# Optimization experiments

Measured on AMD Instinct MI355X. Metric: run time of the kernel, lower is better.

## Reference

```python
import jax, jax.numpy as jnp
import numpy as np

D = 512       # hidden_size (attention defaults hardcode 512)
N = 8         # num_heads
H = D // N    # depth per head = 64
FF = 2048     # FFN filter size (hardcoded)
EPS = 1e-6


def _layer_norm(x, gamma, beta):
    # matches functional layer_norm: biased variance, eps inside sqrt
    mean = jnp.mean(x, axis=-1, keepdims=True)
    var = jnp.mean((x - mean) ** 2, axis=-1, keepdims=True)
    return gamma * ((x - mean) / jnp.sqrt(var + EPS)) + beta


def setup_inputs() -> dict:
    key = jax.random.key(0)
    ks = jax.random.split(key, 12)
    B, S = 8, 1024
    s = lambda k, shape, scale: jax.random.normal(k, shape, jnp.float32) * scale
    return {
        "inputs": s(ks[0], (B, S, D), 1.0),
        "attention_bias": jnp.zeros((B, 1, 1, S), jnp.float32),
        "ln1_g": jnp.ones((D,), jnp.float32),
        "ln1_b": jnp.zeros((D,), jnp.float32),
        "wq": s(ks[1], (D, N, H), D ** -0.5),
        "wk": s(ks[2], (D, N, H), D ** -0.5),
        "wv": s(ks[3], (D, N, H), D ** -0.5),
        "wo": s(ks[4], (N, H, D), D ** -0.5),
        "ln2_g": jnp.ones((D,), jnp.float32),
        "ln2_b": jnp.zeros((D,), jnp.float32),
        "w1": s(ks[5], (D, FF), D ** -0.5),
        "b1": jnp.zeros((FF,), jnp.float32),
        "w2": s(ks[6], (FF, D), FF ** -0.5),
        "b2": jnp.zeros((D,), jnp.float32),
    }


def reference(inputs, attention_bias, ln1_g, ln1_b, wq, wk, wv, wo,
              ln2_g, ln2_b, w1, b1, w2, b2):
    # --- self-attention block (pre-LN, residual) ---
    y = _layer_norm(inputs, ln1_g, ln1_b)
    q = jnp.einsum('bsd,dnh->bsnh', y, wq) * (H ** -0.5)
    k = jnp.einsum('bsd,dnh->bsnh', y, wk)
    v = jnp.einsum('bsd,dnh->bsnh', y, wv)
    # logits[b,n,f,t] = sum_h k[b,t,n,h] * q[b,f,n,h]
    logits = jnp.einsum('btnh,bfnh->bnft', k, q) + attention_bias
    weights = jax.nn.softmax(logits, axis=3)
    attn = jnp.einsum('bnft,btnh->bfnh', weights, v)
    attn_out = jnp.einsum('bfnh,nhd->bfd', attn, wo)
    x = inputs + attn_out

    # --- FFN block (pre-LN, residual) ---
    y2 = _layer_norm(x, ln2_g, ln2_b)
    h = jax.nn.relu(jnp.einsum('bsd,df->bsf', y2, w1) + b1)
    ffn_out = jnp.einsum('bsf,fd->bsd', h, w2) + b2
    return x + ffn_out
```

## Files before the change

kernel.cpp:

```cpp
#include <hip/hip_runtime.h>
#include <stdint.h>

typedef unsigned short u16;
typedef __attribute__((ext_vector_type(8))) __bf16 bf16x8;
typedef __attribute__((ext_vector_type(2))) __bf16 bf16x2;
typedef __attribute__((ext_vector_type(4))) float f32x4;

__device__ __forceinline__ float bf2f(u16 u) {
    union { unsigned int i; float f; } c; c.i = ((unsigned int)u) << 16; return c.f;
}
__device__ __forceinline__ u16 f2bf_sw(float f) {
    union { float f; unsigned int i; } c; c.f = f;
    unsigned int u = c.i;
    u += 0x7FFFu + ((u >> 16) & 1u);
    return (u16)(u >> 16);
}
__device__ __forceinline__ unsigned f2bf2(float lo, float hi) {
#if __has_builtin(__builtin_amdgcn_cvt_pk_bf16_f32)
    union { bf16x2 v; unsigned u; } c;
    c.v = __builtin_amdgcn_cvt_pk_bf16_f32(lo, hi);
    return c.u;
#else
    return (unsigned)f2bf_sw(lo) | ((unsigned)f2bf_sw(hi) << 16);
#endif
}
__device__ __forceinline__ u16 f2bf(float f) {
#if __has_builtin(__builtin_amdgcn_cvt_pk_bf16_f32)
    return (u16)(f2bf2(f, 0.f) & 0xFFFFu);
#else
    return f2bf_sw(f);
#endif
}
__device__ __forceinline__ bool sniff_f32(const unsigned* probe) {
    return probe && ((*probe & 0xFFFFu) == 0u);
}
__device__ __forceinline__ float lde(const void* p, size_t i, bool isf32) {
    return isf32 ? ((const float*)p)[i] : bf2f(((const u16*)p)[i]);
}
__device__ __forceinline__ void g2lds16(const void* g, void* l) {
    __builtin_amdgcn_global_load_lds(
        (__attribute__((address_space(1))) void*)(uintptr_t)g,
        (__attribute__((address_space(3))) void*)(unsigned int)(uintptr_t)l,
        16, 0, 0);
}

__global__ void prep_weights(const void* __restrict__ wq, const void* __restrict__ wk,
                             const void* __restrict__ wv, const void* __restrict__ wo,
                             const void* __restrict__ w1, const void* __restrict__ w2,
                             u16* __restrict__ wqkvT, u16* __restrict__ woT,
                             u16* __restrict__ w1T, u16* __restrict__ w2T,
                             const unsigned* probe) {
    __shared__ u16 t[32][33];
    const bool isf32 = sniff_f32(probe);
    const int id = blockIdx.x;
    const void* src; u16* dst; int R, C, cb, rb; float scale = 1.f;
    if (id < 1024) {
        const int which = id >> 8, tl = id & 255;
        R = 512; C = 512; cb = (tl & 15) * 32; rb = (tl >> 4) * 32;
        if (which == 0)      { src = wq; dst = wqkvT;              scale = 0.125f; }
        else if (which == 1) { src = wk; dst = wqkvT + 512 * 512; }
        else if (which == 2) { src = wv; dst = wqkvT + 1024 * 512; }
        else                 { src = wo; dst = woT; }
    } else if (id < 2048) {
        const int tl = id - 1024; src = w1; dst = w1T; R = 512; C = 2048;
        cb = (tl & 63) * 32; rb = (tl >> 6) * 32;
    } else {
        const int tl = id - 2048; src = w2; dst = w2T; R = 2048; C = 512;
        cb = (tl & 15) * 32; rb = (tl >> 4) * 32;
    }
    const int tx = threadIdx.x, ty = threadIdx.y;
#pragma unroll
    for (int i = 0; i < 4; i++)
        t[ty + i * 8][tx] = f2bf(lde(src, (size_t)(rb + ty + i * 8) * C + cb + tx, isf32));
    __syncthreads();
#pragma unroll
    for (int i = 0; i < 4; i++) {
        float v = bf2f(t[tx][ty + i * 8]) * scale;
        dst[(size_t)(cb + ty + i * 8) * R + rb + tx] = f2bf(v);
    }
}

__global__ __launch_bounds__(256) void ln_any(const void* __restrict__ x,
                                              const void* __restrict__ gw,
                                              const void* __restrict__ bw,
                                              u16* __restrict__ y,
                                              const unsigned* probe_x,
                                              const unsigned* probe_gb) {
    const bool xf32 = sniff_f32(probe_x);
    const bool gf32 = sniff_f32(probe_gb);
    const int lane = threadIdx.x & 63, wave = threadIdx.x >> 6;
    const int r = blockIdx.x * 4 + wave;
    union U8 { uint4 v; u16 s[8]; };
    float xs[8];
    if (xf32) {
        const float4* xr = (const float4*)((const float*)x + (size_t)r * 512 + lane * 8);
        float4 p0 = xr[0], p1 = xr[1];
        xs[0]=p0.x; xs[1]=p0.y; xs[2]=p0.z; xs[3]=p0.w;
        xs[4]=p1.x; xs[5]=p1.y; xs[6]=p1.z; xs[7]=p1.w;
    } else {
        U8 xu; xu.v = *(const uint4*)((const u16*)x + (size_t)r * 512 + lane * 8);
#pragma unroll
        for (int j = 0; j < 8; j++) xs[j] = bf2f(xu.s[j]);
    }
    float s1 = 0.f, s2 = 0.f;
#pragma unroll
    for (int j = 0; j < 8; j++) { s1 += xs[j]; s2 += xs[j] * xs[j]; }
#pragma unroll
    for (int d = 1; d < 64; d <<= 1) { s1 += __shfl_xor(s1, d); s2 += __shfl_xor(s2, d); }
    const float mean = s1 * (1.f / 512.f);
    const float var = s2 * (1.f / 512.f) - mean * mean;
    const float rstd = rsqrtf(var + 1e-6f);
    float gs[8], bs[8];
    if (gf32) {
        const float4* gr = (const float4*)((const float*)gw + lane * 8);
        const float4* br = (const float4*)((const float*)bw + lane * 8);
        float4 g0 = gr[0], g1 = gr[1], b0 = br[0], b1 = br[1];
        gs[0]=g0.x; gs[1]=g0.y; gs[2]=g0.z; gs[3]=g0.w; gs[4]=g1.x; gs[5]=g1.y; gs[6]=g1.z; gs[7]=g1.w;
        bs[0]=b0.x; bs[1]=b0.y; bs[2]=b0.z; bs[3]=b0.w; bs[4]=b1.x; bs[5]=b1.y; bs[6]=b1.z; bs[7]=b1.w;
    } else {
        U8 gu; gu.v = *(const uint4*)((const u16*)gw + lane * 8);
        U8 bu; bu.v = *(const uint4*)((const u16*)bw + lane * 8);
#pragma unroll
        for (int j = 0; j < 8; j++) { gs[j] = bf2f(gu.s[j]); bs[j] = bf2f(bu.s[j]); }
    }
    uint4 ov;
    float o[8];
#pragma unroll
    for (int j = 0; j < 8; j++) o[j] = gs[j] * ((xs[j] - mean) * rstd) + bs[j];
    ov.x = f2bf2(o[0], o[1]); ov.y = f2bf2(o[2], o[3]);
    ov.z = f2bf2(o[4], o[5]); ov.w = f2bf2(o[6], o[7]);
    *(uint4*)(y + (size_t)r * 512 + lane * 8) = ov;
}

template <int EPI, int TM>
__global__ __launch_bounds__(256, 2) void gemm_bt(const u16* __restrict__ A,
                                                  const u16* __restrict__ Bt,
                                                  const void* __restrict__ bias,
                                                  const void* __restrict__ res,
                                                  void* __restrict__ out,
                                                  u16* __restrict__ out2,
                                                  const unsigned* probe,
                                                  int M, int N, int K) {
    constexpr int ACH = TM / 16;
    constexpr int MI = TM / 32;
    __shared__ __align__(16) u16 lA[2][TM * 32];
    __shared__ __align__(16) u16 lB[2][128 * 32];
    const int tid = threadIdx.x, wave = tid >> 6, lane = tid & 63;
    const int m0 = blockIdx.x * TM, n0 = blockIdx.y * 128;
    const int wm = (wave >> 1) * (TM / 2), wn = (wave & 1) * 64;
    const int row = lane & 15, quad = lane >> 4;
    f32x4 acc[MI][4];
#pragma unroll
    for (int i = 0; i < MI; i++)
#pragma unroll
        for (int j = 0; j < 4; j++) acc[i][j] = (f32x4){0.f, 0.f, 0.f, 0.f};
    const u16* Ab = A + (size_t)m0 * K;
    const u16* Bb = Bt + (size_t)n0 * K;

    auto stage = [&](int buf, int k0) {
#pragma unroll
        for (int c = 0; c < (ACH + 8 + 3) / 4; c++) {
            const int ch = c * 4 + wave;
            if (ch < ACH) {
                const int e = ch * 64 + lane;
                const int r = e >> 2, col = (e & 3) * 8;
                g2lds16(Ab + (size_t)r * K + k0 + col, (char*)lA[buf] + ch * 1024);
            } else if (ch < ACH + 8) {
                const int c2 = ch - ACH;
                const int e = c2 * 64 + lane;
                const int r = e >> 2, col = (e & 3) * 8;
                g2lds16(Bb + (size_t)r * K + k0 + col, (char*)lB[buf] + c2 * 1024);
            }
        }
    };

    stage(0, 0);
    int cur = 0;
    for (int k0 = 0; k0 < K; k0 += 32) {
        __syncthreads();
        if (k0 + 32 < K) stage(cur ^ 1, k0 + 32);
        bf16x8 af[MI], bfr[4];
#pragma unroll
        for (int t = 0; t < MI; t++)
            af[t]  = *(const bf16x8*)(lA[cur] + (wm + t * 16 + row) * 32 + quad * 8);
#pragma unroll
        for (int t = 0; t < 4; t++)
            bfr[t] = *(const bf16x8*)(lB[cur] + (wn + t * 16 + row) * 32 + quad * 8);
#pragma unroll
        for (int i = 0; i < MI; i++)
#pragma unroll
            for (int j = 0; j < 4; j++)
                acc[i][j] = __builtin_amdgcn_mfma_f32_16x16x32_bf16(af[i], bfr[j], acc[i][j], 0, 0, 0);
        cur ^= 1;
    }
    const bool isf32 = sniff_f32(probe);
#pragma unroll
    for (int i = 0; i < MI; i++) {
        const int gm = m0 + wm + i * 16 + quad * 4;
#pragma unroll
        for (int j = 0; j < 4; j++) {
            const int gn = n0 + wn + j * 16 + row;
            float bv = 0.f;
            if (EPI == 2 || EPI == 3) bv = lde(bias, gn, isf32);
#pragma unroll
            for (int r = 0; r < 4; r++) {
                float v = acc[i][j][r];
                const int gmr = gm + r;
                size_t idx = (size_t)gmr * N + gn;
                if (EPI == 1) {
                    ((u16*)out)[idx] = f2bf(v + lde(res, idx, isf32));
                } else if (EPI == 2) {
                    v += bv;
                    ((u16*)out)[idx] = f2bf(v > 0.f ? v : 0.f);
                } else if (EPI == 3) {
                    v += bv + bf2f(((const u16*)res)[idx]);
                    if (isf32) ((float*)out)[idx] = v;
                    else       ((u16*)out)[idx] = f2bf(v);
                } else {
                    if (gn < 1024) {
                        ((u16*)out)[(size_t)gmr * 1024 + gn] = f2bf(v);
                    } else {
                        const int j2 = gn - 1024, n = j2 >> 6, h2 = j2 & 63;
                        const int b = gmr >> 10, t = gmr & 1023;
                        out2[(((size_t)b * 8 + n) * 64 + h2) * 1024 + t] = f2bf(v);
                    }
                }
            }
        }
    }
}

__global__ __launch_bounds__(256, 2) void attn_fused(const u16* __restrict__ qk,
                                                     const u16* __restrict__ vT,
                                                     const void* __restrict__ biasp,
                                                     u16* __restrict__ attn,
                                                     const unsigned* probe) {
    __shared__ __align__(16) u16 lQ[64 * 64];
    __shared__ __align__(16) u16 lK[2][128 * 64];
    __shared__ __align__(16) u16 lV[2][64 * 128];
    const bool isf32 = sniff_f32(probe);
    const int tid = threadIdx.x, wave = tid >> 6, lane = tid & 63;
    const int row = lane & 15, quad = lane >> 4;
    const int bn = blockIdx.x, b = bn >> 3, n = bn & 7;
    const int f0 = blockIdx.y * 64;
    const u16* Qg = qk + (size_t)(b * 1024 + f0) * 1024 + n * 64;
    const u16* Kg = qk + (size_t)(b * 1024) * 1024 + 512 + n * 64;
    const u16* Vg = vT + (size_t)bn * 65536;

    auto stageKV = [&](int buf, int t0) {
#pragma unroll
        for (int j = 0; j < 4; j++) {
            const int ch = wave * 4 + j, e = ch * 64 + lane;
            const int rk = e >> 3, ck = ((e & 7) ^ (rk & 7)) * 8;
            g2lds16(Kg + (size_t)(t0 + rk) * 1024 + ck, (char*)lK[buf] + ch * 1024);
            const int rv = e >> 4, cv = ((e & 15) ^ (rv & 7)) * 8;
            g2lds16(Vg + (size_t)rv * 1024 + t0 + cv, (char*)lV[buf] + ch * 1024);
        }
    };

#pragma unroll
    for (int j = 0; j < 2; j++) {
        const int ch = wave * 2 + j, e = ch * 64 + lane;
        const int rq = e >> 3, cq = ((e & 7) ^ (rq & 7)) * 8;
        g2lds16(Qg + (size_t)rq * 1024 + cq, (char*)lQ + ch * 1024);
    }
    stageKV(0, 0);

    float m_i = -1e30f, l_i = 0.f;
    f32x4 oacc[4];
#pragma unroll
    for (int h = 0; h < 4; h++) oacc[h] = (f32x4){0.f, 0.f, 0.f, 0.f};

    int cur = 0;
    for (int t0 = 0; t0 < 1024; t0 += 128) {
        __syncthreads();
        if (t0 + 128 < 1024) stageKV(cur ^ 1, t0 + 128);
        const u16* lKc = lK[cur];
        const u16* lVc = lV[cur];
        f32x4 s[8];
#pragma unroll
        for (int nt = 0; nt < 8; nt++) s[nt] = (f32x4){0.f, 0.f, 0.f, 0.f};
        const int fr = wave * 16 + row;
        bf16x8 bq[2];
#pragma unroll
        for (int ks = 0; ks < 2; ks++)
            bq[ks] = *(const bf16x8*)(lQ + fr * 64 + (((ks * 4 + quad) ^ (fr & 7)) * 8));
#pragma unroll
        for (int nt = 0; nt < 8; nt++) {
            const int tr = nt * 16 + row;
#pragma unroll
            for (int ks = 0; ks < 2; ks++) {
                bf16x8 ak = *(const bf16x8*)(lKc + tr * 64 + (((ks * 4 + quad) ^ (tr & 7)) * 8));
                s[nt] = __builtin_amdgcn_mfma_f32_16x16x32_bf16(ak, bq[ks], s[nt], 0, 0, 0);
            }
        }
        float mx = -1e30f;
#pragma unroll
        for (int nt = 0; nt < 8; nt++) {
            const size_t bidx = (size_t)b * 1024 + t0 + nt * 16 + quad * 4;
            float bv4[4];
            if (isf32) {
                float4 t4 = *(const float4*)((const float*)biasp + bidx);
                bv4[0] = t4.x; bv4[1] = t4.y; bv4[2] = t4.z; bv4[3] = t4.w;
            } else {
                union { uint2 v; u16 s[4]; } bu;
                bu.v = *(const uint2*)((const u16*)biasp + bidx);
#pragma unroll
                for (int r = 0; r < 4; r++) bv4[r] = bf2f(bu.s[r]);
            }
#pragma unroll
            for (int r = 0; r < 4; r++) {
                s[nt][r] += bv4[r];
                mx = fmaxf(mx, s[nt][r]);
            }
        }
        mx = fmaxf(mx, __shfl_xor(mx, 16));
        mx = fmaxf(mx, __shfl_xor(mx, 32));
        const float mn = fmaxf(m_i, mx);
        const float alpha = __expf(m_i - mn);
        float rs = 0.f;
#pragma unroll
        for (int nt = 0; nt < 8; nt++)
#pragma unroll
            for (int r = 0; r < 4; r++) {
                float p = __expf(s[nt][r] - mn);
                s[nt][r] = p;
                rs += p;
            }
        rs += __shfl_xor(rs, 16);
        rs += __shfl_xor(rs, 32);
        l_i = l_i * alpha + rs;
        m_i = mn;
#pragma unroll
        for (int h = 0; h < 4; h++)
#pragma unroll
            for (int r = 0; r < 4; r++) oacc[h][r] *= alpha;
#pragma unroll
        for (int ks = 0; ks < 4; ks++) {
            unsigned pw[4];
#pragma unroll
            for (int g = 0; g < 2; g++) {
                pw[g * 2 + 0] = f2bf2(s[ks * 2 + g][0], s[ks * 2 + g][1]);
                pw[g * 2 + 1] = f2bf2(s[ks * 2 + g][2], s[ks * 2 + g][3]);
            }
            union { unsigned u[4]; bf16x8 v8; } bb;
#pragma unroll
            for (int w = 0; w < 4; w++) {
                const int srcl = ((((quad & 1) << 1) | (w >> 1)) << 4) | row;
                const unsigned lo = (unsigned)__shfl((int)pw[(w & 1)], srcl);
                const unsigned hi = (unsigned)__shfl((int)pw[2 + (w & 1)], srcl);
                bb.u[w] = (quad & 2) ? hi : lo;
            }
#pragma unroll
            for (int ht = 0; ht < 4; ht++) {
                const int vr = ht * 16 + row;
                bf16x8 av = *(const bf16x8*)(lVc + vr * 128 + (((ks * 4 + quad) ^ (vr & 7)) * 8));
                oacc[ht] = __builtin_amdgcn_mfma_f32_16x16x32_bf16(av, bb.v8, oacc[ht], 0, 0, 0);
            }
        }
        cur ^= 1;
    }
    const float inv = 1.f / l_i;
    const int f = f0 + wave * 16 + row;
#pragma unroll
    for (int ht = 0; ht < 4; ht++) {
        uint2 ov;
        ov.x = f2bf2(oacc[ht][0] * inv, oacc[ht][1] * inv);
        ov.y = f2bf2(oacc[ht][2] * inv, oacc[ht][3] * inv);
        *(uint2*)(attn + (size_t)(b * 1024 + f) * 512 + n * 64 + ht * 16 + quad * 4) = ov;
    }
}

extern "C" void kernel_launch(void* const* d_in, const int* in_sizes, int n_in,
                              void* d_out, int out_size, void* d_ws, size_t ws_size,
                              hipStream_t stream) {
    const void* inp  = d_in[0];
    const void* ab   = d_in[1];
    const void* ln1g = d_in[2];
    const void* ln1b = d_in[3];
    const void* wq   = d_in[4];
    const void* wk   = d_in[5];
    const void* wv   = d_in[6];
    const void* wo   = d_in[7];
    const void* ln2g = d_in[8];
    const void* ln2b = d_in[9];
    const void* w1   = d_in[10];
    const void* b1   = d_in[11];
    const void* w2   = d_in[12];
    const void* b2   = d_in[13];
    const unsigned* probe = (const unsigned*)d_in[2];

    char* ws = (char*)d_ws;
    size_t off = 0;
    auto alloc = [&](size_t bytes) -> void* { void* p = ws + off; off += bytes; return p; };
    u16* wqkvT = (u16*)alloc(1536 * 512 * 2);
    u16* woT   = (u16*)alloc(512 * 512 * 2);
    u16* w1T   = (u16*)alloc(2048 * 512 * 2);
    u16* w2T   = (u16*)alloc(512 * 2048 * 2);
    u16* ybuf  = (u16*)alloc((size_t)8192 * 512 * 2);
    u16* qk    = (u16*)alloc((size_t)8192 * 1024 * 2);
    u16* vT    = (u16*)alloc((size_t)64 * 64 * 1024 * 2);
    u16* attn  = (u16*)alloc((size_t)8192 * 512 * 2);
    u16* xbf   = (u16*)alloc((size_t)8192 * 512 * 2);
    u16* hbuf  = qk;

    prep_weights<<<3072, dim3(32, 8), 0, stream>>>(wq, wk, wv, wo, w1, w2,
                                                   wqkvT, woT, w1T, w2T, probe);
    ln_any<<<2048, 256, 0, stream>>>(inp, ln1g, ln1b, ybuf, probe, probe);
    gemm_bt<4, 128><<<dim3(64, 12), 256, 0, stream>>>(ybuf, wqkvT, nullptr, nullptr, qk, vT, nullptr, 8192, 1536, 512);
    attn_fused<<<dim3(64, 16), 256, 0, stream>>>(qk, vT, ab, attn, probe);
    gemm_bt<1, 64><<<dim3(128, 4), 256, 0, stream>>>(attn, woT, nullptr, inp, xbf, nullptr, probe, 8192, 512, 512);
    ln_any<<<2048, 256, 0, stream>>>(xbf, ln2g, ln2b, ybuf, nullptr, probe);
    gemm_bt<2, 128><<<dim3(64, 16), 256, 0, stream>>>(ybuf, w1T, b1, nullptr, hbuf, nullptr, probe, 8192, 2048, 512);
    gemm_bt<3, 64><<<dim3(128, 4), 256, 0, stream>>>(hbuf, w2T, b2, xbf, (u16*)d_out, nullptr, probe, 8192, 512, 2048);
}
```

Baseline: 267.7 us.

## Process two query tiles per wave in attention, single-buffer K/V, cache bias in LDS

The attention kernel now handles 128 query rows per block (32 per wave as two 16-row sub-tiles), so each K and V fragment read from LDS feeds two MFMAs and the grid shrinks to half as many blocks. K/V double buffering is removed in favour of a single buffer with a sync after the load, and the per-batch bias is staged once into LDS as floats instead of being reloaded from global memory each tile. This cuts LDS and global traffic per FLOP, but it exposes the K/V load latency that the prefetch used to hide, raises register pressure (launch bounds changed to 3 blocks), and halves the number of blocks (512 on the GPU).

```diff
diff --git a/kernel.cpp b/kernel.cpp
--- a/kernel.cpp
+++ b/kernel.cpp
@@ -230,144 +230,162 @@
     }
 }
 
-__global__ __launch_bounds__(256, 2) void attn_fused(const u16* __restrict__ qk,
+__global__ __launch_bounds__(256, 3) void attn_fused(const u16* __restrict__ qk,
                                                      const u16* __restrict__ vT,
                                                      const void* __restrict__ biasp,
                                                      u16* __restrict__ attn,
                                                      const unsigned* probe) {
-    __shared__ __align__(16) u16 lQ[64 * 64];
-    __shared__ __align__(16) u16 lK[2][128 * 64];
-    __shared__ __align__(16) u16 lV[2][64 * 128];
+    __shared__ __align__(16) u16 lQ[128 * 64];
+    __shared__ __align__(16) u16 lK[128 * 64];
+    __shared__ __align__(16) u16 lV[64 * 128];
+    __shared__ __align__(16) float lBias[1024];
     const bool isf32 = sniff_f32(probe);
     const int tid = threadIdx.x, wave = tid >> 6, lane = tid & 63;
     const int row = lane & 15, quad = lane >> 4;
     const int bn = blockIdx.x, b = bn >> 3, n = bn & 7;
-    const int f0 = blockIdx.y * 64;
+    const int f0 = blockIdx.y * 128;
     const u16* Qg = qk + (size_t)(b * 1024 + f0) * 1024 + n * 64;
     const u16* Kg = qk + (size_t)(b * 1024) * 1024 + 512 + n * 64;
     const u16* Vg = vT + (size_t)bn * 65536;
 
-    auto stageKV = [&](int buf, int t0) {
+#pragma unroll
+    for (int j = 0; j < 4; j++) {
+        const int ch = wave * 4 + j, e = ch * 64 + lane;
+        const int rq = e >> 3, cq = ((e & 7) ^ (rq & 7)) * 8;
+        g2lds16(Qg + (size_t)rq * 1024 + cq, (char*)lQ + ch * 1024);
+    }
+    {
+        const int i4 = tid * 4;
+        if (isf32) {
+            *(float4*)(lBias + i4) = *(const float4*)((const float*)biasp + (size_t)b * 1024 + i4);
+        } else {
+            union { uint2 v; u16 s[4]; } bu;
+            bu.v = *(const uint2*)((const u16*)biasp + (size_t)b * 1024 + i4);
+            float4 t4 = {bf2f(bu.s[0]), bf2f(bu.s[1]), bf2f(bu.s[2]), bf2f(bu.s[3])};
+            *(float4*)(lBias + i4) = t4;
+        }
+    }
+
+    float m_i[2] = {-1e30f, -1e30f}, l_i[2] = {0.f, 0.f};
+    f32x4 oacc[2][4];
+#pragma unroll
+    for (int a = 0; a < 2; a++)
+#pragma unroll
+        for (int h = 0; h < 4; h++) oacc[a][h] = (f32x4){0.f, 0.f, 0.f, 0.f};
+
+    for (int t0 = 0; t0 < 1024; t0 += 128) {
+        __syncthreads();
 #pragma unroll
         for (int j = 0; j < 4; j++) {
             const int ch = wave * 4 + j, e = ch * 64 + lane;
             const int rk = e >> 3, ck = ((e & 7) ^ (rk & 7)) * 8;
-            g2lds16(Kg + (size_t)(t0 + rk) * 1024 + ck, (char*)lK[buf] + ch * 1024);
+            g2lds16(Kg + (size_t)(t0 + rk) * 1024 + ck, (char*)lK + ch * 1024);
             const int rv = e >> 4, cv = ((e & 15) ^ (rv & 7)) * 8;
-            g2lds16(Vg + (size_t)rv * 1024 + t0 + cv, (char*)lV[buf] + ch * 1024);
-        }
-    };
-
-#pragma unroll
-    for (int j = 0; j < 2; j++) {
-        const int ch = wave * 2 + j, e = ch * 64 + lane;
-        const int rq = e >> 3, cq = ((e & 7) ^ (rq & 7)) * 8;
-        g2lds16(Qg + (size_t)rq * 1024 + cq, (char*)lQ + ch * 1024);
-    }
-    stageKV(0, 0);
-
-    float m_i = -1e30f, l_i = 0.f;
-    f32x4 oacc[4];
-#pragma unroll
-    for (int h = 0; h < 4; h++) oacc[h] = (f32x4){0.f, 0.f, 0.f, 0.f};
-
-    int cur = 0;
-    for (int t0 = 0; t0 < 1024; t0 += 128) {
+            g2lds16(Vg + (size_t)rv * 1024 + t0 + cv, (char*)lV + ch * 1024);
+        }
         __syncthreads();
-        if (t0 + 128 < 1024) stageKV(cur ^ 1, t0 + 128);
-        const u16* lKc = lK[cur];
-        const u16* lVc = lV[cur];
-        f32x4 s[8];
-#pragma unroll
-        for (int nt = 0; nt < 8; nt++) s[nt] = (f32x4){0.f, 0.f, 0.f, 0.f};
-        const int fr = wave * 16 + row;
-        bf16x8 bq[2];
-#pragma unroll
-        for (int ks = 0; ks < 2; ks++)
-            bq[ks] = *(const bf16x8*)(lQ + fr * 64 + (((ks * 4 + quad) ^ (fr & 7)) * 8));
+        f32x4 s[2][8];
+#pragma unroll
+        for (int a = 0; a < 2; a++)
+#pragma unroll
+            for (int nt = 0; nt < 8; nt++) s[a][nt] = (f32x4){0.f, 0.f, 0.f, 0.f};
+        bf16x8 bq[2][2];
+#pragma unroll
+        for (int a = 0; a < 2; a++) {
+            const int fr = wave * 32 + a * 16 + row;
+#pragma unroll
+            for (int ks = 0; ks < 2; ks++)
+                bq[a][ks] = *(const bf16x8*)(lQ + fr * 64 + (((ks * 4 + quad) ^ (fr & 7)) * 8));
+        }
 #pragma unroll
         for (int nt = 0; nt < 8; nt++) {
             const int tr = nt * 16 + row;
 #pragma unroll
             for (int ks = 0; ks < 2; ks++) {
-                bf16x8 ak = *(const bf16x8*)(lKc + tr * 64 + (((ks * 4 + quad) ^ (tr & 7)) * 8));
-                s[nt] = __builtin_amdgcn_mfma_f32_16x16x32_bf16(ak, bq[ks], s[nt], 0, 0, 0);
+                bf16x8 ak = *(const bf16x8*)(lK + tr * 64 + (((ks * 4 + quad) ^ (tr & 7)) * 8));
+#pragma unroll
+                for (int a = 0; a < 2; a++)
+                    s[a][nt] = __builtin_amdgcn_mfma_f32_16x16x32_bf16(ak, bq[a][ks], s[a][nt], 0, 0, 0);
             }
         }
-        float mx = -1e30f;
+        float bv4[8][4];
 #pragma unroll
         for (int nt = 0; nt < 8; nt++) {
-            const size_t bidx = (size_t)b * 1024 + t0 + nt * 16 + quad * 4;
-            float bv4[4];
-            if (isf32) {
-                float4 t4 = *(const float4*)((const float*)biasp + bidx);
-                bv4[0] = t4.x; bv4[1] = t4.y; bv4[2] = t4.z; bv4[3] = t4.w;
-            } else {
-                union { uint2 v; u16 s[4]; } bu;
-                bu.v = *(const uint2*)((const u16*)biasp + bidx);
-#pragma unroll
-                for (int r = 0; r < 4; r++) bv4[r] = bf2f(bu.s[r]);
-            }
-#pragma unroll
-            for (int r = 0; r < 4; r++) {
-                s[nt][r] += bv4[r];
-                mx = fmaxf(mx, s[nt][r]);
-            }
-        }
-        mx = fmaxf(mx, __shfl_xor(mx, 16));
-        mx = fmaxf(mx, __shfl_xor(mx, 32));
-        const float mn = fmaxf(m_i, mx);
-        const float alpha = __expf(m_i - mn);
-        float rs = 0.f;
-#pragma unroll
-        for (int nt = 0; nt < 8; nt++)
-#pragma unroll
-            for (int r = 0; r < 4; r++) {
-                float p = __expf(s[nt][r] - mn);
-                s[nt][r] = p;
-                rs += p;
-            }
-        rs += __shfl_xor(rs, 16);
-        rs += __shfl_xor(rs, 32);
-        l_i = l_i * alpha + rs;
-        m_i = mn;
-#pragma unroll
-        for (int h = 0; h < 4; h++)
-#pragma unroll
-            for (int r = 0; r < 4; r++) oacc[h][r] *= alpha;
+            float4 t4 = *(const float4*)(lBias + t0 + nt * 16 + quad * 4);
+            bv4[nt][0] = t4.x; bv4[nt][1] = t4.y; bv4[nt][2] = t4.z; bv4[nt][3] = t4.w;
+        }
+#pragma unroll
+        for (int a = 0; a < 2; a++) {
+            float mx = -1e30f;
+#pragma unroll
+            for (int nt = 0; nt < 8; nt++)
+#pragma unroll
+                for (int r = 0; r < 4; r++) {
+                    s[a][nt][r] += bv4[nt][r];
+                    mx = fmaxf(mx, s[a][nt][r]);
+                }
+            mx = fmaxf(mx, __shfl_xor(mx, 16));
+            mx = fmaxf(mx, __shfl_xor(mx, 32));
+            const float mn = fmaxf(m_i[a], mx);
+            const float alpha = __expf(m_i[a] - mn);
+            float rs = 0.f;
+#pragma unroll
+            for (int nt = 0; nt < 8; nt++)
+#pragma unroll
+                for (int r = 0; r < 4; r++) {
+                    float p = __expf(s[a][nt][r] - mn);
+                    s[a][nt][r] = p;
+                    rs += p;
+                }
+            rs += __shfl_xor(rs, 16);
+            rs += __shfl_xor(rs, 32);
+            l_i[a] = l_i[a] * alpha + rs;
+            m_i[a] = mn;
+#pragma unroll
+            for (int h = 0; h < 4; h++)
+#pragma unroll
+                for (int r = 0; r < 4; r++) oacc[a][h][r] *= alpha;
+        }
 #pragma unroll
         for (int ks = 0; ks < 4; ks++) {
-            unsigned pw[4];
-#pragma unroll
-            for (int g = 0; g < 2; g++) {
-                pw[g * 2 + 0] = f2bf2(s[ks * 2 + g][0], s[ks * 2 + g][1]);
-                pw[g * 2 + 1] = f2bf2(s[ks * 2 + g][2], s[ks * 2 + g][3]);
-            }
-            union { unsigned u[4]; bf16x8 v8; } bb;
-#pragma unroll
-            for (int w = 0; w < 4; w++) {
-                const int srcl = ((((quad & 1) << 1) | (w >> 1)) << 4) | row;
-                const unsigned lo = (unsigned)__shfl((int)pw[(w & 1)], srcl);
-                const unsigned hi = (unsigned)__shfl((int)pw[2 + (w & 1)], srcl);
-                bb.u[w] = (quad & 2) ? hi : lo;
+            union { unsigned u[4]; bf16x8 v8; } bb[2];
+#pragma unroll
+            for (int a = 0; a < 2; a++) {
+                unsigned pw[4];
+#pragma unroll
+                for (int g = 0; g < 2; g++) {
+                    pw[g * 2 + 0] = f2bf2(s[a][ks * 2 + g][0], s[a][ks * 2 + g][1]);
+                    pw[g * 2 + 1] = f2bf2(s[a][ks * 2 + g][2], s[a][ks * 2 + g][3]);
+                }
+#pragma unroll
+                for (int w = 0; w < 4; w++) {
+                    const int srcl = ((((quad & 1) << 1) | (w >> 1)) << 4) | row;
+                    const unsigned lo = (unsigned)__shfl((int)pw[(w & 1)], srcl);
+                    const unsigned hi = (unsigned)__shfl((int)pw[2 + (w & 1)], srcl);
+                    bb[a].u[w] = (quad & 2) ? hi : lo;
+                }
             }
 #pragma unroll
             for (int ht = 0; ht < 4; ht++) {
                 const int vr = ht * 16 + row;
-                bf16x8 av = *(const bf16x8*)(lVc + vr * 128 + (((ks * 4 + quad) ^ (vr & 7)) * 8));
-                oacc[ht] = __builtin_amdgcn_mfma_f32_16x16x32_bf16(av, bb.v8, oacc[ht], 0, 0, 0);
+                bf16x8 av = *(const bf16x8*)(lV + vr * 128 + (((ks * 4 + quad) ^ (vr & 7)) * 8));
+#pragma unroll
+                for (int a = 0; a < 2; a++)
+                    oacc[a][ht] = __builtin_amdgcn_mfma_f32_16x16x32_bf16(av, bb[a].v8, oacc[a][ht], 0, 0, 0);
             }
         }
-        cur ^= 1;
-    }
-    const float inv = 1.f / l_i;
-    const int f = f0 + wave * 16 + row;
-#pragma unroll
-    for (int ht = 0; ht < 4; ht++) {
-        uint2 ov;
-        ov.x = f2bf2(oacc[ht][0] * inv, oacc[ht][1] * inv);
-        ov.y = f2bf2(oacc[ht][2] * inv, oacc[ht][3] * inv);
-        *(uint2*)(attn + (size_t)(b * 1024 + f) * 512 + n * 64 + ht * 16 + quad * 4) = ov;
+    }
+#pragma unroll
+    for (int a = 0; a < 2; a++) {
+        const float inv = 1.f / l_i[a];
+        const int f = f0 + wave * 32 + a * 16 + row;
+#pragma unroll
+        for (int ht = 0; ht < 4; ht++) {
+            uint2 ov;
+            ov.x = f2bf2(oacc[a][ht][0] * inv, oacc[a][ht][1] * inv);
+            ov.y = f2bf2(oacc[a][ht][2] * inv, oacc[a][ht][3] * inv);
+            *(uint2*)(attn + (size_t)(b * 1024 + f) * 512 + n * 64 + ht * 16 + quad * 4) = ov;
+        }
     }
 }
 
@@ -408,7 +426,7 @@
                                                    wqkvT, woT, w1T, w2T, probe);
     ln_any<<<2048, 256, 0, stream>>>(inp, ln1g, ln1b, ybuf, probe, probe);
     gemm_bt<4, 128><<<dim3(64, 12), 256, 0, stream>>>(ybuf, wqkvT, nullptr, nullptr, qk, vT, nullptr, 8192, 1536, 512);
-    attn_fused<<<dim3(64, 16), 256, 0, stream>>>(qk, vT, ab, attn, probe);
+    attn_fused<<<dim3(64, 8), 256, 0, stream>>>(qk, vT, ab, attn, probe);
     gemm_bt<1, 64><<<dim3(128, 4), 256, 0, stream>>>(attn, woT, nullptr, inp, xbf, nullptr, probe, 8192, 512, 512);
     ln_any<<<2048, 256, 0, stream>>>(xbf, ln2g, ln2b, ybuf, nullptr, probe);
     gemm_bt<2, 128><<<dim3(64, 16), 256, 0, stream>>>(ybuf, w1T, b1, nullptr, hbuf, nullptr, probe, 8192, 2048, 512);
```

After: 265.1 us. About the same (-1.0%).
